# Kernel tuning notes

Measured on AMD Instinct MI355X. Metric: run time of the kernel, lower is better.

## Reference

```python
import jax, jax.numpy as jnp
import numpy as np

B, C, D, H = 32, 512, 512, 8  # batch, enc_in channels, d_model, num_heads
W = D // H                    # per-head width in frequency domain
BN_EPS = 1e-5


def _lin(k, din, dout):
    # weight stored as [in, out]; apply as x @ W + b (equivalent to torch Linear)
    return jax.random.normal(k, (din, dout), jnp.float32) / np.sqrt(din)


def setup_inputs() -> dict:
    key = jax.random.key(0)
    ks = jax.random.split(key, 16)
    return {
        "x": jax.random.normal(ks[0], (B, C, D), jnp.float32),
        "W_in": _lin(ks[1], D, D), "b_in": jnp.zeros((D,), jnp.float32),
        "W_q": _lin(ks[2], D, D), "b_q": jnp.zeros((D,), jnp.float32),
        "W_k": _lin(ks[3], D, D), "b_k": jnp.zeros((D,), jnp.float32),
        "W_v": _lin(ks[4], D, D), "b_v": jnp.zeros((D,), jnp.float32),
        "temperature": jnp.ones((H, 1), jnp.float32),
        "W1a": _lin(ks[5], D, D), "b1a": jnp.zeros((D,), jnp.float32),
        "bn_gamma": jnp.ones((C,), jnp.float32),
        "bn_beta": jnp.zeros((C,), jnp.float32),
        "bn_mean": 0.1 * jax.random.normal(ks[6], (C,), jnp.float32),
        "bn_var": 1.0 + 0.1 * jax.random.uniform(ks[7], (C,), jnp.float32),
        "W1b": _lin(ks[8], D, D), "b1b": jnp.zeros((D,), jnp.float32),
        "W_out": _lin(ks[9], 2 * D, D), "b_out": jnp.zeros((D,), jnp.float32),
    }


def _complex_l2_normalize(z):
    # torch F.normalize on complex: divide by L2 norm of |z| along last dim
    n = jnp.sqrt(jnp.sum(jnp.abs(z) ** 2, axis=-1, keepdims=True))
    return z / jnp.maximum(n, 1e-12)


def reference(x, W_in, b_in, W_q, b_q, W_k, b_k, W_v, b_v, temperature,
              W1a, b1a, bn_gamma, bn_beta, bn_mean, bn_var, W1b, b1b,
              W_out, b_out):
    b, c, d = x.shape
    h, w = H, d // H

    conv2 = x @ W_in + b_in                       # in_projector (dropout = identity, eval)
    q = conv2 @ W_q + b_q
    k = conv2 @ W_k + b_k
    v = conv2 @ W_v + b_v

    # 2-D FFT over last two axes (c, d), as torch.fft.fft2 does on [b, c, d]
    q_f = jnp.fft.fft2(q).reshape(b, c, h, w)
    k_f = jnp.fft.fft2(k).reshape(b, c, h, w)
    v_f = jnp.fft.fft2(v).reshape(b, c, h, w)
    tep = jnp.fft.fft2(conv2)                     # [b, c, d] complex

    q_f = _complex_l2_normalize(q_f)
    k_f = _complex_l2_normalize(k_f)

    # [b, c, h, h] complex attention scores, scaled by real (8,1) temperature
    attn = jnp.einsum('bchw,bcgw->bchg', q_f, k_f) * temperature
    # custom complex softmax: softmax real and imag parts independently
    attn = jax.nn.softmax(attn.real, axis=-1) + 1j * jax.nn.softmax(attn.imag, axis=-1)

    out_f = jnp.einsum('bchg,bcgw->bchw', attn, v_f)        # complex [b,c,h,w]
    out_f = jnp.abs(jnp.fft.ifft2(out_f)).reshape(b, c, d)  # ifft2 over (h,w)

    # gated branch: Linear -> BatchNorm1d(enc_in, eval) -> ReLU -> Linear -> Sigmoid
    g = tep.real @ W1a + b1a
    g = (g - bn_mean[None, :, None]) * jax.lax.rsqrt(bn_var[None, :, None] + BN_EPS)
    g = g * bn_gamma[None, :, None] + bn_beta[None, :, None]
    g = jax.nn.relu(g) @ W1b + b1b
    g = jax.nn.sigmoid(g)
    out_l = jnp.abs(jnp.fft.ifft2(g * tep))                 # [b, c, d]

    out2 = jnp.concatenate([out_f, out_l], axis=-1) @ W_out + b_out
    return out2 + conv2
```

## Files before the change

kernel.cpp:

```cpp
#include <hip/hip_runtime.h>
#include <hip/hip_bf16.h>

#define FFT_PI 3.14159265358979323846f
#define FOFF(i) ((i) + ((i) >> 3))

typedef __hip_bfloat16 bf16;
typedef short bf8_t __attribute__((ext_vector_type(8)));
typedef float f4_t __attribute__((ext_vector_type(4)));

__device__ inline float bf2f(unsigned short u) {
    union { unsigned int i; float f; } v; v.i = ((unsigned int)u) << 16; return v.f;
}
__device__ inline unsigned short f2bf(float f) {
    bf16 h = __float2bfloat16(f);
    union { bf16 h; unsigned short u; } v; v.h = h; return v.u;
}
__device__ inline float2 c_load(const ushort2* p) {
    ushort2 u = *p;
    return make_float2(bf2f(u.x), bf2f(u.y));
}
__device__ inline int brev6(int t) {
    return ((t & 1) << 5) | ((t & 2) << 3) | ((t & 4) << 1) |
           ((t & 8) >> 1) | ((t & 16) >> 3) | ((t & 32) >> 5);
}
__device__ inline float2 cadd(float2 a, float2 b){ return make_float2(a.x+b.x, a.y+b.y); }
__device__ inline float2 csub(float2 a, float2 b){ return make_float2(a.x-b.x, a.y-b.y); }
__device__ inline float2 cmul(float2 a, float2 b){
    return make_float2(a.x*b.x - a.y*b.y, a.x*b.y + a.y*b.x);
}
__device__ inline float2 cmuli(float2 a, float s){ return make_float2(-s*a.y, s*a.x); }

__global__ __launch_bounds__(256) void transpose_cvt_all(
    const float* __restrict__ s0, const float* __restrict__ s1,
    const float* __restrict__ s2, const float* __restrict__ s3,
    const float* __restrict__ s4, const float* __restrict__ s5,
    const float* __restrict__ s6, bf16* __restrict__ Wt)
{
    const int z = blockIdx.z;
    const int R = (z == 6) ? 1024 : 512;
    if (blockIdx.y * 32 >= R) return;
    const float* src = (z == 0) ? s0 : (z == 1) ? s1 : (z == 2) ? s2 :
                       (z == 3) ? s3 : (z == 4) ? s4 : (z == 5) ? s5 : s6;
    bf16* dst = Wt + (long)z * 262144;
    const int C = 512;

    __shared__ float tile[32][33];
    const int bx = blockIdx.x * 32;
    const int by = blockIdx.y * 32;
    const int tx = threadIdx.x, ty = threadIdx.y;
#pragma unroll
    for (int i = 0; i < 32; i += 8)
        tile[ty + i][tx] = src[(long)(by + ty + i) * C + bx + tx];
    __syncthreads();
#pragma unroll
    for (int i = 0; i < 32; i += 8)
        dst[(long)(bx + ty + i) * R + by + tx] = __float2bfloat16(tile[tx][ty + i]);
}

__global__ __launch_bounds__(256) void mfma_gemm(
    const void* __restrict__ Av, const void* __restrict__ Av2,
    int a_type, int lda, int ksplit,
    const bf16* __restrict__ Bt, int ldb,
    const float* __restrict__ bias0, const float* __restrict__ bias1,
    const float* __restrict__ bias2,
    void* __restrict__ C0, void* __restrict__ C1, void* __restrict__ C2,
    int nper, int out_type, int ldc, int K,
    const float* __restrict__ e0, const float* __restrict__ e1,
    const float* __restrict__ e2, const float* __restrict__ e3)
{
    __shared__ short Asub[128 * 40];
    __shared__ short Bsub[128 * 40];

    const int tid = threadIdx.x;
    const int n0 = blockIdx.x * 128;
    const int m0 = blockIdx.y * 128;
    const int l  = tid & 63;
    const int wv = tid >> 6;
    const int wm = wv & 1, wn = wv >> 1;

    f4_t acc[4][4];
#pragma unroll
    for (int i = 0; i < 4; i++)
#pragma unroll
        for (int j = 0; j < 4; j++)
            acc[i][j] = (f4_t)0.f;

    const int srow = tid >> 2;
    const int sc8  = (tid & 3) * 8;

    for (int k0 = 0; k0 < K; k0 += 32) {
        const void* As = (k0 < ksplit) ? Av : Av2;
        const int kk = (k0 < ksplit) ? k0 : (k0 - ksplit);
#pragma unroll
        for (int p = 0; p < 2; p++) {
            const int row = srow + p * 64;
            bf8_t av;
            if (a_type == 0) {
                av = *(const bf8_t*)((const bf16*)As
                    + (long)(m0 + row) * lda + kk + sc8);
            } else if (a_type == 1) {
                const float4* src = (const float4*)((const float*)As
                    + (long)(m0 + row) * lda + kk + sc8);
                float4 u0 = src[0], u1 = src[1];
                av[0] = (short)f2bf(u0.x); av[1] = (short)f2bf(u0.y);
                av[2] = (short)f2bf(u0.z); av[3] = (short)f2bf(u0.w);
                av[4] = (short)f2bf(u1.x); av[5] = (short)f2bf(u1.y);
                av[6] = (short)f2bf(u1.z); av[7] = (short)f2bf(u1.w);
            } else {
                const ushort2* src = (const ushort2*)As
                    + (long)(m0 + row) * lda + kk + sc8;
#pragma unroll
                for (int j = 0; j < 8; j++) av[j] = (short)src[j].x;
            }
            *(bf8_t*)&Asub[row * 40 + sc8] = av;

            bf8_t bv = *(const bf8_t*)(Bt + (long)(n0 + row) * ldb + k0 + sc8);
            *(bf8_t*)&Bsub[row * 40 + sc8] = bv;
        }
        __syncthreads();

        bf8_t a_frag[4], b_frag[4];
        const int ko = (l >> 4) * 8;
        const int lr = l & 15;
#pragma unroll
        for (int fm = 0; fm < 4; fm++)
            a_frag[fm] = *(bf8_t*)&Asub[(wm * 64 + fm * 16 + lr) * 40 + ko];
#pragma unroll
        for (int fn = 0; fn < 4; fn++)
            b_frag[fn] = *(bf8_t*)&Bsub[(wn * 64 + fn * 16 + lr) * 40 + ko];
#pragma unroll
        for (int fm = 0; fm < 4; fm++)
#pragma unroll
            for (int fn = 0; fn < 4; fn++)
                acc[fm][fn] = __builtin_amdgcn_mfma_f32_16x16x32_bf16(
                    b_frag[fn], a_frag[fm], acc[fm][fn], 0, 0, 0);
        __syncthreads();
    }

    const int sel = n0 / nper;
    const int nb  = sel * nper;
    const float* biasl = (sel == 0) ? bias0 : ((sel == 1) ? bias1 : bias2);
    void* Cl = (sel == 0) ? C0 : ((sel == 1) ? C1 : C2);

    const int em = m0 + wm * 64 + (l & 15);
    const int en = n0 + wn * 64 + ((l >> 4) << 2);
#pragma unroll
    for (int fm = 0; fm < 4; fm++) {
        const long m = em + fm * 16;
        float bnm = 0.f, bnr = 1.f, bng = 1.f, bnb = 0.f;
        if (out_type == 3) {
            const int c = (int)(m & 511);
            bnm = e0[c];
            bnr = 1.0f / sqrtf(e1[c] + 1e-5f);
            bng = e2[c];
            bnb = e3[c];
        }
#pragma unroll
        for (int fn = 0; fn < 4; fn++) {
            const int n = en + fn * 16;
            const int nl = n - nb;
            f4_t v = acc[fm][fn];
            if (biasl) {
#pragma unroll
                for (int r = 0; r < 4; r++) v[r] += biasl[nl + r];
            }
            if (out_type == 0) {
                float4 o; o.x = v[0]; o.y = v[1]; o.z = v[2]; o.w = v[3];
                *(float4*)((float*)Cl + m * ldc + nl) = o;
            } else if (out_type == 1) {
                union { unsigned short u[4]; ushort4 q; } o;
#pragma unroll
                for (int r = 0; r < 4; r++) o.u[r] = f2bf(v[r]);
                *(ushort4*)((bf16*)Cl + m * ldc + nl) = o.q;
            } else if (out_type == 2) {
                union { ushort2 u2[4]; uint4 q; } o;
#pragma unroll
                for (int r = 0; r < 4; r++) { o.u2[r].x = f2bf(v[r]); o.u2[r].y = 0; }
                *(uint4*)((ushort2*)Cl + m * ldc + nl) = o.q;
            } else if (out_type == 3) {
                union { unsigned short u[4]; ushort4 q; } o;
#pragma unroll
                for (int r = 0; r < 4; r++)
                    o.u[r] = f2bf(fmaxf((v[r] - bnm) * bnr * bng + bnb, 0.f));
                *(ushort4*)((bf16*)Cl + m * ldc + nl) = o.q;
            } else {
                union { unsigned short u[4]; ushort4 q; } rsd;
                rsd.q = *(const ushort4*)((const unsigned short*)e0 + m * ldc + nl);
                float4 o;
                o.x = v[0] + bf2f(rsd.u[0]);
                o.y = v[1] + bf2f(rsd.u[1]);
                o.z = v[2] + bf2f(rsd.u[2]);
                o.w = v[3] + bf2f(rsd.u[3]);
                *(float4*)((float*)Cl + m * ldc + nl) = o;
            }
        }
    }
}

__device__ inline void dft8(float2* x, float sgn)
{
    const float c45 = 0.70710678118654752f;
    float2 e0, e1, e2, e3, o0, o1, o2, o3;
    {
        float2 u0 = cadd(x[0], x[4]), u1 = csub(x[0], x[4]);
        float2 u2 = cadd(x[2], x[6]), u3 = cmuli(csub(x[2], x[6]), sgn);
        e0 = cadd(u0, u2); e1 = cadd(u1, u3); e2 = csub(u0, u2); e3 = csub(u1, u3);
    }
    {
        float2 u0 = cadd(x[1], x[5]), u1 = csub(x[1], x[5]);
        float2 u2 = cadd(x[3], x[7]), u3 = cmuli(csub(x[3], x[7]), sgn);
        o0 = cadd(u0, u2); o1 = cadd(u1, u3); o2 = csub(u0, u2); o3 = csub(u1, u3);
    }
    const float2 w1 = make_float2(c45, sgn * c45);
    const float2 w3 = make_float2(-c45, sgn * c45);
    o1 = cmul(o1, w1);
    o2 = cmuli(o2, sgn);
    o3 = cmul(o3, w3);
    x[0] = cadd(e0, o0); x[4] = csub(e0, o0);
    x[1] = cadd(e1, o1); x[5] = csub(e1, o1);
    x[2] = cadd(e2, o2); x[6] = csub(e2, o2);
    x[3] = cadd(e3, o3); x[7] = csub(e3, o3);
}

__device__ inline void fft512_r8(float2* bx0, float2* by0, int lane, float sign)
{
    float2* bx = bx0;
    float2* by = by0;
#pragma unroll
    for (int st = 0; st < 3; st++) {
        int n, m, sstr, p, q;
        if (st == 0)      { n = 512; m = 64; sstr = 1;  p = lane;      q = 0; }
        else if (st == 1) { n = 64;  m = 8;  sstr = 8;  p = lane >> 3; q = lane & 7; }
        else              { n = 8;   m = 1;  sstr = 64; p = 0;         q = lane; }
        float2 x[8];
#pragma unroll
        for (int r = 0; r < 8; r++) x[r] = bx[FOFF(q + sstr * (p + r * m))];
        dft8(x, sign);
        if (p) {
            float ang = sign * (2.0f * FFT_PI) * (float)p / (float)n;
            float sw, cw;
            __sincosf(ang, &sw, &cw);
            float2 w = make_float2(cw, sw), wk = w;
#pragma unroll
            for (int k = 1; k < 8; k++) { x[k] = cmul(x[k], wk); wk = cmul(wk, w); }
        }
#pragma unroll
        for (int k = 0; k < 8; k++) by[FOFF(q + sstr * (8 * p + k))] = x[k];
        __syncthreads();
        float2* t = bx; bx = by; by = t;
    }
}

__global__ __launch_bounds__(256) void fft8_rows_c2c3(
    ushort2* __restrict__ data, float sign)
{
    __shared__ float2 B0[4][576], B1[4][576];
    const int buf = blockIdx.x >> 12;
    const int lb  = blockIdx.x & 4095;
    const int li = threadIdx.x >> 6, lane = threadIdx.x & 63;
    ushort2* s = data + (long)buf * 8388608 + ((long)lb * 4 + li) * 512;
    {
        uint4 r0 = *(const uint4*)(s + lane * 8);
        uint4 r1 = *(const uint4*)(s + lane * 8 + 4);
        float2* dst = &B0[li][9 * lane];
        const ushort2* pp = (const ushort2*)&r0;
#pragma unroll
        for (int j = 0; j < 4; j++) dst[j] = c_load(pp + j);
        pp = (const ushort2*)&r1;
#pragma unroll
        for (int j = 0; j < 4; j++) dst[4 + j] = c_load(pp + j);
    }
    __syncthreads();
    fft512_r8(B0[li], B1[li], lane, sign);
    {
        float2* src = &B1[li][9 * lane];
        union { ushort2 u[4]; uint4 q; } o0, o1;
#pragma unroll
        for (int j = 0; j < 4; j++) {
            float2 z = src[j]; o0.u[j].x = f2bf(z.x); o0.u[j].y = f2bf(z.y);
        }
#pragma unroll
        for (int j = 0; j < 4; j++) {
            float2 z = src[4 + j]; o1.u[j].x = f2bf(z.x); o1.u[j].y = f2bf(z.y);
        }
        *(uint4*)(s + lane * 8) = o0.q;
        *(uint4*)(s + lane * 8 + 4) = o1.q;
    }
}

__global__ __launch_bounds__(256) void fft8_rows_r2c(
    const bf16* __restrict__ srcb, ushort2* __restrict__ dst)
{
    __shared__ float2 B0[4][576], B1[4][576];
    const int li = threadIdx.x >> 6, lane = threadIdx.x & 63;
    const long line = (long)blockIdx.x * 4 + li;
    {
        uint4 raw = *(const uint4*)((const unsigned short*)srcb + line * 512 + lane * 8);
        const unsigned short* pp = (const unsigned short*)&raw;
        float2* d = &B0[li][9 * lane];
#pragma unroll
        for (int j = 0; j < 8; j++) d[j] = make_float2(bf2f(pp[j]), 0.f);
    }
    __syncthreads();
    fft512_r8(B0[li], B1[li], lane, -1.f);
    {
        ushort2* s = dst + line * 512;
        float2* src = &B1[li][9 * lane];
        union { ushort2 u[4]; uint4 q; } o0, o1;
#pragma unroll
        for (int j = 0; j < 4; j++) {
            float2 z = src[j]; o0.u[j].x = f2bf(z.x); o0.u[j].y = f2bf(z.y);
        }
#pragma unroll
        for (int j = 0; j < 4; j++) {
            float2 z = src[4 + j]; o1.u[j].x = f2bf(z.x); o1.u[j].y = f2bf(z.y);
        }
        *(uint4*)(s + lane * 8) = o0.q;
        *(uint4*)(s + lane * 8 + 4) = o1.q;
    }
}

__global__ __launch_bounds__(256) void fft8_rows_gated(
    const bf16* __restrict__ g2, ushort2* __restrict__ tep)
{
    __shared__ float2 B0[4][576], B1[4][576];
    const int li = threadIdx.x >> 6, lane = threadIdx.x & 63;
    const long line = (long)blockIdx.x * 4 + li;
    ushort2* s = tep + line * 512;
    {
        uint4 rg = *(const uint4*)((const unsigned short*)g2 + line * 512 + lane * 8);
        uint4 r0 = *(const uint4*)(s + lane * 8);
        uint4 r1 = *(const uint4*)(s + lane * 8 + 4);
        const unsigned short* gp = (const unsigned short*)&rg;
        float2* d = &B0[li][9 * lane];
        const ushort2* pp = (const ushort2*)&r0;
#pragma unroll
        for (int j = 0; j < 4; j++) {
            float sg = 1.0f / (1.0f + __expf(-bf2f(gp[j])));
            float2 z = c_load(pp + j);
            d[j] = make_float2(sg * z.x, sg * z.y);
        }
        pp = (const ushort2*)&r1;
#pragma unroll
        for (int j = 0; j < 4; j++) {
            float sg = 1.0f / (1.0f + __expf(-bf2f(gp[4 + j])));
            float2 z = c_load(pp + j);
            d[4 + j] = make_float2(sg * z.x, sg * z.y);
        }
    }
    __syncthreads();
    fft512_r8(B0[li], B1[li], lane, +1.f);
    {
        const float sc = 1.0f / 512.0f;
        float2* src = &B1[li][9 * lane];
        union { ushort2 u[4]; uint4 q; } o0, o1;
#pragma unroll
        for (int j = 0; j < 4; j++) {
            float2 z = src[j];
            o0.u[j].x = f2bf(z.x * sc); o0.u[j].y = f2bf(z.y * sc);
        }
#pragma unroll
        for (int j = 0; j < 4; j++) {
            float2 z = src[4 + j];
            o1.u[j].x = f2bf(z.x * sc); o1.u[j].y = f2bf(z.y * sc);
        }
        *(uint4*)(s + lane * 8) = o0.q;
        *(uint4*)(s + lane * 8 + 4) = o1.q;
    }
}

__global__ __launch_bounds__(256) void fft8_cols16_c2c4(
    ushort2* __restrict__ data, bf16* __restrict__ tepReal, float sign)
{
    __shared__ float2 B[512][16];
    const int buf = blockIdx.x >> 10;
    const int rem = blockIdx.x & 1023;
    const int b   = rem >> 5;
    const int c0  = (rem & 31) * 16;
    ushort2* base = data + (long)buf * 8388608 + (long)b * 262144 + c0;
    const int t = threadIdx.x;
    const int lr = t >> 2;
    const int lq = t & 3;

#pragma unroll
    for (int it = 0; it < 8; it++) {
        const int row = it * 64 + lr;
        uint4 raw = *(const uint4*)(base + (long)row * 512 + lq * 4);
        const ushort2* pp = (const ushort2*)&raw;
#pragma unroll
        for (int j = 0; j < 4; j++) B[row][lq * 4 + j] = c_load(pp + j);
    }
    __syncthreads();

    const int col = t & 15;
    const int rb  = t >> 4;
#pragma unroll
    for (int st = 0; st < 3; st++) {
        int n, m, s;
        if (st == 0)      { n = 512; m = 64; s = 1;  }
        else if (st == 1) { n = 64;  m = 8;  s = 8;  }
        else              { n = 8;   m = 1;  s = 64; }
        float2 x[4][8];
        int ps[4], qs[4];
#pragma unroll
        for (int i = 0; i < 4; i++) {
            const int role = rb + 16 * i;
            int p, q;
            if (st == 0)      { p = role;      q = 0; }
            else if (st == 1) { p = role >> 3; q = role & 7; }
            else              { p = 0;         q = role; }
            ps[i] = p; qs[i] = q;
#pragma unroll
            for (int r = 0; r < 8; r++)
                x[i][r] = B[q + s * (p + r * m)][col];
        }
        __syncthreads();
#pragma unroll
        for (int i = 0; i < 4; i++) {
            dft8(x[i], sign);
            const int p = ps[i];
            if (p) {
                float ang = sign * (2.0f * FFT_PI) * (float)p / (float)n;
                float sw, cw;
                __sincosf(ang, &sw, &cw);
                float2 w = make_float2(cw, sw), wk = w;
#pragma unroll
                for (int k = 1; k < 8; k++) { x[i][k] = cmul(x[i][k], wk); wk = cmul(wk, w); }
            }
#pragma unroll
            for (int k = 0; k < 8; k++)
                B[qs[i] + s * (8 * p + k)][col] = x[i][k];
        }
        __syncthreads();
    }

#pragma unroll
    for (int it = 0; it < 8; it++) {
        const int row = it * 64 + lr;
        union { ushort2 u[4]; uint4 q4; } o;
        union { unsigned short u[4]; ushort4 q4; } orl;
#pragma unroll
        for (int j = 0; j < 4; j++) {
            float2 z = B[row][lq * 4 + j];
            o.u[j].x = f2bf(z.x); o.u[j].y = f2bf(z.y);
            orl.u[j] = o.u[j].x;
        }
        *(uint4*)(base + (long)row * 512 + lq * 4) = o.q4;
        if (buf == 3)
            *(ushort4*)(tepReal + (long)b * 262144 + (long)row * 512 + c0 + lq * 4) = orl.q4;
    }
}

__global__ __launch_bounds__(256) void fft8_cols16_abs(
    const ushort2* __restrict__ src, bf16* __restrict__ dst)
{
    __shared__ float2 B[512][16];
    const int b  = blockIdx.x >> 5;
    const int c0 = (blockIdx.x & 31) * 16;
    const ushort2* base = src + (long)b * 262144 + c0;
    const int t = threadIdx.x;
    const int lr = t >> 2;
    const int lq = t & 3;

#pragma unroll
    for (int it = 0; it < 8; it++) {
        const int row = it * 64 + lr;
        uint4 raw = *(const uint4*)(base + (long)row * 512 + lq * 4);
        const ushort2* pp = (const ushort2*)&raw;
#pragma unroll
        for (int j = 0; j < 4; j++) B[row][lq * 4 + j] = c_load(pp + j);
    }
    __syncthreads();

    const int col = t & 15;
    const int rb  = t >> 4;
#pragma unroll
    for (int st = 0; st < 3; st++) {
        int n, m, s;
        if (st == 0)      { n = 512; m = 64; s = 1;  }
        else if (st == 1) { n = 64;  m = 8;  s = 8;  }
        else              { n = 8;   m = 1;  s = 64; }
        float2 x[4][8];
        int ps[4], qs[4];
#pragma unroll
        for (int i = 0; i < 4; i++) {
            const int role = rb + 16 * i;
            int p, q;
            if (st == 0)      { p = role;      q = 0; }
            else if (st == 1) { p = role >> 3; q = role & 7; }
            else              { p = 0;         q = role; }
            ps[i] = p; qs[i] = q;
#pragma unroll
            for (int r = 0; r < 8; r++)
                x[i][r] = B[q + s * (p + r * m)][col];
        }
        __syncthreads();
#pragma unroll
        for (int i = 0; i < 4; i++) {
            dft8(x[i], +1.f);
            const int p = ps[i];
            if (p) {
                float ang = (2.0f * FFT_PI) * (float)p / (float)n;
                float sw, cw;
                __sincosf(ang, &sw, &cw);
                float2 w = make_float2(cw, sw), wk = w;
#pragma unroll
                for (int k = 1; k < 8; k++) { x[i][k] = cmul(x[i][k], wk); wk = cmul(wk, w); }
            }
#pragma unroll
            for (int k = 0; k < 8; k++)
                B[qs[i] + s * (8 * p + k)][col] = x[i][k];
        }
        __syncthreads();
    }

    const float sc = 1.0f / 512.0f;
#pragma unroll
    for (int it = 0; it < 8; it++) {
        const int row = it * 64 + lr;
        union { unsigned short u[4]; ushort4 q4; } o;
#pragma unroll
        for (int j = 0; j < 4; j++) {
            float2 z = B[row][lq * 4 + j];
            o.u[j] = f2bf(sqrtf(z.x * z.x + z.y * z.y) * sc);
        }
        *(ushort4*)(dst + (long)b * 262144 + (long)row * 512 + c0 + lq * 4) = o.q4;
    }
}

__global__ __launch_bounds__(256) void attn_kernel(
    const ushort2* __restrict__ qf, const ushort2* __restrict__ kf,
    const ushort2* __restrict__ vf, const float* __restrict__ temp,
    bf16* __restrict__ out_f)
{
    __shared__ float2 QS[4][8][66];
    __shared__ float2 KS[4][8][66];
    __shared__ float2 ATT[4][8][9];

    const int li = threadIdx.x >> 6, lane = threadIdx.x & 63;
    const int bc = blockIdx.x * 4 + li;
    const long base = (long)bc * 512;

    float2 q[8], k[8], v[8];
#pragma unroll
    for (int h = 0; h < 8; h++) {
        q[h] = c_load(qf + base + h * 64 + lane);
        k[h] = c_load(kf + base + h * 64 + lane);
        v[h] = c_load(vf + base + h * 64 + lane);
    }

#pragma unroll
    for (int h = 0; h < 8; h++) {
        float pq = q[h].x * q[h].x + q[h].y * q[h].y;
        float pk = k[h].x * k[h].x + k[h].y * k[h].y;
#pragma unroll
        for (int o = 32; o > 0; o >>= 1) {
            pq += __shfl_xor(pq, o, 64);
            pk += __shfl_xor(pk, o, 64);
        }
        float iq = 1.0f / fmaxf(sqrtf(pq), 1e-12f);
        float ik = 1.0f / fmaxf(sqrtf(pk), 1e-12f);
        q[h].x *= iq; q[h].y *= iq;
        k[h].x *= ik; k[h].y *= ik;
        QS[li][h][lane] = q[h];
        KS[li][h][lane] = k[h];
    }
    __syncthreads();

    {
        const int h = lane >> 3, g = lane & 7;
        float ar = 0.f, ai = 0.f;
#pragma unroll 8
        for (int w = 0; w < 64; w += 2) {
            float4 aa = *(const float4*)&QS[li][h][w];
            float4 bb = *(const float4*)&KS[li][g][w];
            ar += aa.x * bb.x - aa.y * bb.y + aa.z * bb.z - aa.w * bb.w;
            ai += aa.x * bb.y + aa.y * bb.x + aa.z * bb.w + aa.w * bb.z;
        }
        float tm = temp[h];
        ATT[li][h][g] = make_float2(ar * tm, ai * tm);
    }
    __syncthreads();

    if (lane < 8) {
        const int h = lane;
        float mr = -1e30f, mi = -1e30f;
        for (int g = 0; g < 8; g++) {
            mr = fmaxf(mr, ATT[li][h][g].x);
            mi = fmaxf(mi, ATT[li][h][g].y);
        }
        float er[8], ei[8];
        float sr = 0.f, si = 0.f;
        for (int g = 0; g < 8; g++) {
            er[g] = __expf(ATT[li][h][g].x - mr); sr += er[g];
            ei[g] = __expf(ATT[li][h][g].y - mi); si += ei[g];
        }
        float isr = 1.f / sr, isi = 1.f / si;
        for (int g = 0; g < 8; g++)
            ATT[li][h][g] = make_float2(er[g] * isr, ei[g] * isi);
    }
    __syncthreads();

    float2 o[8];
#pragma unroll
    for (int h = 0; h < 8; h++) {
        float orr = 0.f, oi = 0.f;
#pragma unroll
        for (int g = 0; g < 8; g++) {
            float2 a = ATT[li][h][g], b = v[g];
            orr += a.x * b.x - a.y * b.y;
            oi  += a.x * b.y + a.y * b.x;
        }
        o[h] = make_float2(orr, oi);
    }

#pragma unroll
    for (int m = 32; m >= 1; m >>= 1) {
        float ang = (FFT_PI / (float)m) * (float)(lane & (m - 1));
        float sw, cw;
        __sincosf(ang, &sw, &cw);
        const bool low = (lane & m) == 0;
#pragma unroll
        for (int h = 0; h < 8; h++) {
            float px = __shfl_xor(o[h].x, m, 64);
            float py = __shfl_xor(o[h].y, m, 64);
            float nx, ny;
            if (low) {
                nx = o[h].x + px;
                ny = o[h].y + py;
            } else {
                float dx = px - o[h].x;
                float dy = py - o[h].y;
                nx = dx * cw - dy * sw;
                ny = dx * sw + dy * cw;
            }
            o[h].x = nx; o[h].y = ny;
        }
    }
    const int wr = brev6(lane);

    const float r2 = 0.70710678118654752f;
    const float W8x[8] = {1.f,  r2, 0.f, -r2, -1.f, -r2,  0.f,  r2};
    const float W8y[8] = {0.f,  r2, 1.f,  r2,  0.f, -r2, -1.f, -r2};
    unsigned short* stg = (unsigned short*)&QS[li][0][0];
#pragma unroll
    for (int kh = 0; kh < 8; kh++) {
        float sr = 0.f, si = 0.f;
#pragma unroll
        for (int n = 0; n < 8; n++) {
            const int idx = (n * kh) & 7;
            float wx = W8x[idx], wy = W8y[idx];
            sr += o[n].x * wx - o[n].y * wy;
            si += o[n].x * wy + o[n].y * wx;
        }
        stg[kh * 64 + wr] = f2bf(sqrtf(sr * sr + si * si) * (1.0f / 512.0f));
    }
    __syncthreads();
    uint4 ov = *(uint4*)(stg + lane * 8);
    *(uint4*)((unsigned short*)out_f + base + lane * 8) = ov;
}

extern "C" void kernel_launch(void* const* d_in, const int* in_sizes, int n_in,
                              void* d_out, int out_size, void* d_ws, size_t ws_size,
                              hipStream_t stream)
{
    const float* x     = (const float*)d_in[0];
    const float* W_in  = (const float*)d_in[1];
    const float* b_in  = (const float*)d_in[2];
    const float* W_q   = (const float*)d_in[3];
    const float* b_q   = (const float*)d_in[4];
    const float* W_k   = (const float*)d_in[5];
    const float* b_k   = (const float*)d_in[6];
    const float* W_v   = (const float*)d_in[7];
    const float* b_v   = (const float*)d_in[8];
    const float* temp  = (const float*)d_in[9];
    const float* W1a   = (const float*)d_in[10];
    const float* b1a   = (const float*)d_in[11];
    const float* gam   = (const float*)d_in[12];
    const float* bet   = (const float*)d_in[13];
    const float* mea   = (const float*)d_in[14];
    const float* var   = (const float*)d_in[15];
    const float* W1b   = (const float*)d_in[16];
    const float* b1b   = (const float*)d_in[17];
    const float* W_out = (const float*)d_in[18];
    const float* b_out = (const float*)d_in[19];

    char* wsb = (char*)d_ws;
    const long MB = 1024 * 1024;
    bf16*    conv2b  = (bf16*)wsb;
    bf16*    tepReal = (bf16*)(wsb + 16 * MB);
    ushort2* Qb    = (ushort2*)(wsb + 32 * MB);
    ushort2* Kb    = (ushort2*)(wsb + 64 * MB);
    ushort2* Vb    = (ushort2*)(wsb + 96 * MB);
    ushort2* Tb    = (ushort2*)(wsb + 128 * MB);
    bf16*    Wt    = (bf16*)(wsb + 160 * MB);
    bf16* WT_in  = Wt;
    bf16* WT_q   = Wt + 262144;
    bf16* WT_1a  = Wt + 4 * 262144;
    bf16* WT_1b  = Wt + 5 * 262144;
    bf16* WT_out = Wt + 6 * 262144;
    bf16* outF = (bf16*)Qb;
    bf16* g1b  = (bf16*)Kb;
    bf16* outL = (bf16*)Kb;
    bf16* g2b  = (bf16*)Vb;

    const dim3 ggrid(4, 128), gblk(256);
    const int BIG = 1 << 30;
    const int RB = 4096;

    transpose_cvt_all<<<dim3(16, 32, 7), dim3(32, 8), 0, stream>>>(
        W_in, W_q, W_k, W_v, W1a, W1b, W_out, Wt);

    mfma_gemm<<<ggrid, gblk, 0, stream>>>(
        x, x, 1, 512, BIG, WT_in, 512, b_in, nullptr, nullptr,
        conv2b, nullptr, nullptr, BIG, 1, 512, 512,
        nullptr, nullptr, nullptr, nullptr);

    mfma_gemm<<<dim3(12, 128), gblk, 0, stream>>>(
        conv2b, conv2b, 0, 512, BIG, WT_q, 512, b_q, b_k, b_v,
        Qb, Kb, Vb, 512, 2, 512, 512,
        nullptr, nullptr, nullptr, nullptr);

    fft8_rows_c2c3<<<3 * RB, 256, 0, stream>>>(Qb, -1.f);
    fft8_rows_r2c<<<RB, 256, 0, stream>>>(conv2b, Tb);

    fft8_cols16_c2c4<<<4096, 256, 0, stream>>>(Qb, tepReal, -1.f);

    attn_kernel<<<RB, 256, 0, stream>>>(Qb, Kb, Vb, temp, outF);

    mfma_gemm<<<ggrid, gblk, 0, stream>>>(
        tepReal, tepReal, 0, 512, BIG, WT_1a, 512, b1a, nullptr, nullptr,
        g1b, nullptr, nullptr, BIG, 3, 512, 512,
        mea, var, gam, bet);

    mfma_gemm<<<ggrid, gblk, 0, stream>>>(
        g1b, g1b, 0, 512, BIG, WT_1b, 512, b1b, nullptr, nullptr,
        g2b, nullptr, nullptr, BIG, 1, 512, 512,
        nullptr, nullptr, nullptr, nullptr);

    fft8_rows_gated<<<RB, 256, 0, stream>>>(g2b, Tb);
    fft8_cols16_abs<<<1024, 256, 0, stream>>>(Tb, outL);

    mfma_gemm<<<ggrid, gblk, 0, stream>>>(
        outF, outL, 0, 512, 512, WT_out, 1024, b_out, nullptr, nullptr,
        d_out, nullptr, nullptr, BIG, 4, 512, 1024,
        (const float*)conv2b, nullptr, nullptr, nullptr);
}
```

Baseline: 569.5 us.

## Async LDS loads in GEMM, merge row FFT kernels, shuffle-based softmax

The GEMM now stages A (bf16 case) and B tiles straight from global memory into LDS with global_load_lds, and drops the padded 40-short row stride for an unpadded 32-short layout. The three-buffer complex row FFT and the real-to-complex row FFT are merged into one launch that branches on block index. The attention softmax is now computed across 8 lanes with xor shuffles instead of a serial pass by 8 threads behind an extra barrier. Dropping the padding may cause LDS bank conflicts on fragment reads, and the a_type==2 path has been removed.

New measurement: 538.9 us. 1.06x faster.

```diff
diff --git a/kernel.cpp b/kernel.cpp
--- a/kernel.cpp
+++ b/kernel.cpp
@@ -29,6 +29,12 @@
     return make_float2(a.x*b.x - a.y*b.y, a.x*b.y + a.y*b.x);
 }
 __device__ inline float2 cmuli(float2 a, float s){ return make_float2(-s*a.y, s*a.x); }
+
+__device__ inline void async_load16(const void* gp, void* lp) {
+    __builtin_amdgcn_global_load_lds(
+        (const __attribute__((address_space(1))) void*)gp,
+        (__attribute__((address_space(3))) void*)lp, 16, 0, 0);
+}
 
 __global__ __launch_bounds__(256) void transpose_cvt_all(
     const float* __restrict__ s0, const float* __restrict__ s1,
@@ -68,8 +74,8 @@
     const float* __restrict__ e0, const float* __restrict__ e1,
     const float* __restrict__ e2, const float* __restrict__ e3)
 {
-    __shared__ short Asub[128 * 40];
-    __shared__ short Bsub[128 * 40];
+    __shared__ short Asub[128 * 32];
+    __shared__ short Bsub[128 * 32];
 
     const int tid = threadIdx.x;
     const int n0 = blockIdx.x * 128;
@@ -85,37 +91,46 @@
         for (int j = 0; j < 4; j++)
             acc[i][j] = (f4_t)0.f;
 
-    const int srow = tid >> 2;
-    const int sc8  = (tid & 3) * 8;
+    const int crow = l >> 2;
+    const int cpc  = (l & 3) * 8;
 
     for (int k0 = 0; k0 < K; k0 += 32) {
         const void* As = (k0 < ksplit) ? Av : Av2;
         const int kk = (k0 < ksplit) ? k0 : (k0 - ksplit);
-#pragma unroll
-        for (int p = 0; p < 2; p++) {
-            const int row = srow + p * 64;
-            bf8_t av;
-            if (a_type == 0) {
-                av = *(const bf8_t*)((const bf16*)As
-                    + (long)(m0 + row) * lda + kk + sc8);
-            } else if (a_type == 1) {
+
+        if (a_type == 0) {
+#pragma unroll
+            for (int c = 0; c < 2; c++) {
+                const int chunk = wv * 2 + c;
+                const int row = chunk * 16 + crow;
+                async_load16((const bf16*)As + (long)(m0 + row) * lda + kk + cpc,
+                             &Asub[chunk * 512]);
+                async_load16(Bt + (long)(n0 + row) * ldb + k0 + cpc,
+                             &Bsub[chunk * 512]);
+            }
+        } else {
+            const int srow = tid >> 2;
+            const int sc8  = (tid & 3) * 8;
+#pragma unroll
+            for (int p = 0; p < 2; p++) {
+                const int row = srow + p * 64;
                 const float4* src = (const float4*)((const float*)As
                     + (long)(m0 + row) * lda + kk + sc8);
                 float4 u0 = src[0], u1 = src[1];
+                bf8_t av;
                 av[0] = (short)f2bf(u0.x); av[1] = (short)f2bf(u0.y);
                 av[2] = (short)f2bf(u0.z); av[3] = (short)f2bf(u0.w);
                 av[4] = (short)f2bf(u1.x); av[5] = (short)f2bf(u1.y);
                 av[6] = (short)f2bf(u1.z); av[7] = (short)f2bf(u1.w);
-            } else {
-                const ushort2* src = (const ushort2*)As
-                    + (long)(m0 + row) * lda + kk + sc8;
-#pragma unroll
-                for (int j = 0; j < 8; j++) av[j] = (short)src[j].x;
+                *(bf8_t*)&Asub[row * 32 + sc8] = av;
             }
-            *(bf8_t*)&Asub[row * 40 + sc8] = av;
-
-            bf8_t bv = *(const bf8_t*)(Bt + (long)(n0 + row) * ldb + k0 + sc8);
-            *(bf8_t*)&Bsub[row * 40 + sc8] = bv;
+#pragma unroll
+            for (int c = 0; c < 2; c++) {
+                const int chunk = wv * 2 + c;
+                const int row = chunk * 16 + crow;
+                async_load16(Bt + (long)(n0 + row) * ldb + k0 + cpc,
+                             &Bsub[chunk * 512]);
+            }
         }
         __syncthreads();
 
@@ -124,10 +139,10 @@
         const int lr = l & 15;
 #pragma unroll
         for (int fm = 0; fm < 4; fm++)
-            a_frag[fm] = *(bf8_t*)&Asub[(wm * 64 + fm * 16 + lr) * 40 + ko];
+            a_frag[fm] = *(bf8_t*)&Asub[(wm * 64 + fm * 16 + lr) * 32 + ko];
 #pragma unroll
         for (int fn = 0; fn < 4; fn++)
-            b_frag[fn] = *(bf8_t*)&Bsub[(wn * 64 + fn * 16 + lr) * 40 + ko];
+            b_frag[fn] = *(bf8_t*)&Bsub[(wn * 64 + fn * 16 + lr) * 32 + ko];
 #pragma unroll
         for (int fm = 0; fm < 4; fm++)
 #pragma unroll
@@ -251,15 +266,18 @@
     }
 }
 
-__global__ __launch_bounds__(256) void fft8_rows_c2c3(
-    ushort2* __restrict__ data, float sign)
+__global__ __launch_bounds__(256) void fft8_rows_all(
+    ushort2* __restrict__ qkv, const bf16* __restrict__ conv2,
+    ushort2* __restrict__ tb)
 {
     __shared__ float2 B0[4][576], B1[4][576];
     const int buf = blockIdx.x >> 12;
     const int lb  = blockIdx.x & 4095;
     const int li = threadIdx.x >> 6, lane = threadIdx.x & 63;
-    ushort2* s = data + (long)buf * 8388608 + ((long)lb * 4 + li) * 512;
-    {
+    const long line = (long)lb * 4 + li;
+
+    if (buf < 3) {
+        ushort2* s = qkv + (long)buf * 8388608 + line * 512;
         uint4 r0 = *(const uint4*)(s + lane * 8);
         uint4 r1 = *(const uint4*)(s + lane * 8 + 4);
         float2* dst = &B0[li][9 * lane];
@@ -269,10 +287,8 @@
         pp = (const ushort2*)&r1;
 #pragma unroll
         for (int j = 0; j < 4; j++) dst[4 + j] = c_load(pp + j);
-    }
-    __syncthreads();
-    fft512_r8(B0[li], B1[li], lane, sign);
-    {
+        __syncthreads();
+        fft512_r8(B0[li], B1[li], lane, -1.f);
         float2* src = &B1[li][9 * lane];
         union { ushort2 u[4]; uint4 q; } o0, o1;
 #pragma unroll
@@ -285,26 +301,15 @@
         }
         *(uint4*)(s + lane * 8) = o0.q;
         *(uint4*)(s + lane * 8 + 4) = o1.q;
-    }
-}
-
-__global__ __launch_bounds__(256) void fft8_rows_r2c(
-    const bf16* __restrict__ srcb, ushort2* __restrict__ dst)
-{
-    __shared__ float2 B0[4][576], B1[4][576];
-    const int li = threadIdx.x >> 6, lane = threadIdx.x & 63;
-    const long line = (long)blockIdx.x * 4 + li;
-    {
-        uint4 raw = *(const uint4*)((const unsigned short*)srcb + line * 512 + lane * 8);
+    } else {
+        uint4 raw = *(const uint4*)((const unsigned short*)conv2 + line * 512 + lane * 8);
         const unsigned short* pp = (const unsigned short*)&raw;
         float2* d = &B0[li][9 * lane];
 #pragma unroll
         for (int j = 0; j < 8; j++) d[j] = make_float2(bf2f(pp[j]), 0.f);
-    }
-    __syncthreads();
-    fft512_r8(B0[li], B1[li], lane, -1.f);
-    {
-        ushort2* s = dst + line * 512;
+        __syncthreads();
+        fft512_r8(B0[li], B1[li], lane, -1.f);
+        ushort2* s = tb + line * 512;
         float2* src = &B1[li][9 * lane];
         union { ushort2 u[4]; uint4 q; } o0, o1;
 #pragma unroll
@@ -578,26 +583,21 @@
             ai += aa.x * bb.y + aa.y * bb.x + aa.z * bb.w + aa.w * bb.z;
         }
         float tm = temp[h];
-        ATT[li][h][g] = make_float2(ar * tm, ai * tm);
-    }
-    __syncthreads();
-
-    if (lane < 8) {
-        const int h = lane;
-        float mr = -1e30f, mi = -1e30f;
-        for (int g = 0; g < 8; g++) {
-            mr = fmaxf(mr, ATT[li][h][g].x);
-            mi = fmaxf(mi, ATT[li][h][g].y);
-        }
-        float er[8], ei[8];
-        float sr = 0.f, si = 0.f;
-        for (int g = 0; g < 8; g++) {
-            er[g] = __expf(ATT[li][h][g].x - mr); sr += er[g];
-            ei[g] = __expf(ATT[li][h][g].y - mi); si += ei[g];
-        }
-        float isr = 1.f / sr, isi = 1.f / si;
-        for (int g = 0; g < 8; g++)
-            ATT[li][h][g] = make_float2(er[g] * isr, ei[g] * isi);
+        ar *= tm; ai *= tm;
+        float mr = ar, mi = ai;
+#pragma unroll
+        for (int o = 1; o < 8; o <<= 1) {
+            mr = fmaxf(mr, __shfl_xor(mr, o, 64));
+            mi = fmaxf(mi, __shfl_xor(mi, o, 64));
+        }
+        float er = __expf(ar - mr), ei = __expf(ai - mi);
+        float sr = er, si = ei;
+#pragma unroll
+        for (int o = 1; o < 8; o <<= 1) {
+            sr += __shfl_xor(sr, o, 64);
+            si += __shfl_xor(si, o, 64);
+        }
+        ATT[li][h][g] = make_float2(er / sr, ei / si);
     }
     __syncthreads();
 
@@ -721,8 +721,7 @@
         Qb, Kb, Vb, 512, 2, 512, 512,
         nullptr, nullptr, nullptr, nullptr);
 
-    fft8_rows_c2c3<<<3 * RB, 256, 0, stream>>>(Qb, -1.f);
-    fft8_rows_r2c<<<RB, 256, 0, stream>>>(conv2b, Tb);
+    fft8_rows_all<<<4 * RB, 256, 0, stream>>>(Qb, conv2b, Tb);
 
     fft8_cols16_c2c4<<<4096, 256, 0, stream>>>(Qb, tepReal, -1.f);
 
```
